# Kernel optimization log

Measured on AMD Instinct MI355X. Metric: run time of the kernel, lower is better.

The kernel has to match this reference:

```python
import jax, jax.numpy as jnp
import numpy as np
from functools import partial

EPS = 1e-10


@partial(jax.custom_vjp, nondiff_argnums=(1,))
def kwta(x, k):
    # k-WTA: keep top-k values along last dim, zero elsewhere (STE backward).
    vals, _ = jax.lax.top_k(x, k)
    thresh = vals[..., -1:]
    return jnp.where(x >= thresh, x, jnp.zeros((), x.dtype))


def _kwta_fwd(x, k):
    out = kwta(x, k)
    mask = (out != 0).astype(x.dtype)  # matches torch: mask = (out != 0)
    return out, mask


def _kwta_bwd(k, mask, g):
    return (g * mask,)


kwta.defvjp(_kwta_fwd, _kwta_bwd)


def _sparsify(x, W_down, k):
    h = jax.nn.relu(x @ W_down.T)          # (B, T, N_ca3)
    h = kwta(h, k)
    norm = jnp.maximum(jnp.linalg.norm(h, axis=-1, keepdims=True), EPS)
    return h / norm


def _retrieve_successor(sparse, W_ca3, k):
    # retrieval_steps = 1; replicate the early-break on all-zero activity.
    h = jax.nn.relu(sparse @ W_ca3.T)       # (B, T, N_ca3)
    valid = h.sum() >= EPS
    hk = kwta(h, k)
    norm = jnp.maximum(jnp.linalg.norm(hk, axis=-1, keepdims=True), EPS)
    return jnp.where(valid, hk / norm, sparse)


def setup_inputs() -> dict:
    key = jax.random.key(0)
    k1, k2, k3, k4, k5, k6 = jax.random.split(key, 6)
    B, T, D, N = 4, 2048, 1024, 4096
    x = jax.random.normal(k1, (B, T, D), dtype=jnp.float32)
    # xavier_normal: std = gain * sqrt(2 / (fan_in + fan_out))
    W_down = jax.random.normal(k2, (N, D), dtype=jnp.float32) * (0.5 * np.sqrt(2.0 / (D + N)))
    W_up = jax.random.normal(k3, (D, N), dtype=jnp.float32) * (0.1 * np.sqrt(2.0 / (D + N)))
    # gate_proj weight is zero-init in torch; use small random for a nontrivial gate
    W_gate = jax.random.normal(k4, (D, D), dtype=jnp.float32) * 0.02
    b_gate = jnp.full((D,), -2.0, dtype=jnp.float32)
    # W_ca3 buffer is zero-init then Hebbian-learned; random stand-in
    W_ca3 = jax.random.normal(k6, (N, N), dtype=jnp.float32) * 0.02
    return {"x": x, "W_down": W_down, "W_up": W_up, "W_gate": W_gate,
            "b_gate": b_gate, "W_ca3": W_ca3, "k": 64}


def reference(x, W_down, W_up, W_gate, b_gate, W_ca3, k):
    sparse = _sparsify(x, W_down, k)                    # (B, T, N)
    successor = _retrieve_successor(sparse, W_ca3, k)   # (B, T, N)
    prediction = successor @ W_up.T                     # (B, T, D)
    g = jax.nn.sigmoid(x @ W_gate.T + b_gate)           # (B, T, D)
    return x + g * prediction
```

## Files before the change

kernel.cpp:

```cpp
#include <hip/hip_runtime.h>
#include <hip/hip_bf16.h>
#include <stdint.h>

typedef float f32x4 __attribute__((ext_vector_type(4)));
typedef int i32x4 __attribute__((ext_vector_type(4)));

#define MROWS 8192
#define DD 1024
#define DN 4096

__device__ __forceinline__ void load_lds16(const void* g, void* l) {
  __builtin_amdgcn_global_load_lds((const __attribute__((address_space(1))) void*)g,
                                   (__attribute__((address_space(3))) void*)l, 16, 0, 0);
}

template<int EPI>
__global__ void __launch_bounds__(512, 1)
gemm_i8_8ph(const uint8_t* __restrict__ A, const uint8_t* __restrict__ B,
            __hip_bfloat16* __restrict__ Cb, int M, int N, int K,
            float* __restrict__ vsum,
            const float* __restrict__ sA, const float* __restrict__ sB)
{
  extern __shared__ __align__(16) char smem[];
  const int tid  = threadIdx.x;
  const int lane = tid & 63;
  const int wave = tid >> 6;
  const int wm = wave >> 2;
  const int wn = wave & 3;

  const int nwg = gridDim.x;
  const int bid = ((int)blockIdx.x % 8) * (nwg >> 3) + ((int)blockIdx.x >> 3);

  const int nbn = N >> 8;
  const int bm = (bid / nbn) << 8;
  const int bn = (bid % nbn) << 8;

  const int NT = K >> 7;

  i32x4 acc[8][4];
  const i32x4 izero = {0, 0, 0, 0};
#pragma unroll
  for (int i = 0; i < 8; ++i)
#pragma unroll
    for (int j = 0; j < 4; ++j)
      acc[i][j] = izero;

  const int csb = (((tid & 3) ^ ((tid >> 3) & 3)) << 4);
  const uint8_t* Ag = A + (size_t)(bm + (tid >> 2)) * K + csb;
  const uint8_t* Bg = B + (size_t)(bn + (tid >> 2)) * K + csb;

  const int rl = lane & 15;
  const int kc = lane >> 4;
  const int chunk_off = ((kc ^ ((rl >> 1) & 3)) << 4);
  const int aoff = ((wm << 7) + rl) * 64 + chunk_off;
  const int boff = ((wn << 6) + rl) * 64 + chunk_off;

#define STAGE_A8(S, KH) do { \
    const int kt_ = (((S) & (NT - 1)) << 7) + ((KH) << 6); \
    char* dst_ = smem + (((((S) & 1) << 1) | (KH)) << 14) + (tid << 4); \
    load_lds16(Ag + kt_, dst_); \
    load_lds16(Ag + (size_t)128 * K + kt_, dst_ + 8192); \
  } while (0)

#define STAGE_B8(S, KH) do { \
    const int kt_ = (((S) & (NT - 1)) << 7) + ((KH) << 6); \
    char* dst_ = smem + 65536 + (((((S) & 1) << 1) | (KH)) << 14) + (tid << 4); \
    load_lds16(Bg + kt_, dst_); \
    load_lds16(Bg + (size_t)128 * K + kt_, dst_ + 8192); \
  } while (0)

  i32x4 afS[2][4];
  i32x4 b0, b1, b2, b3;

#define MFMA_ROW8(MI, AF) \
    acc[MI][0] = __builtin_amdgcn_mfma_i32_16x16x64_i8(AF, b0, acc[MI][0], 0, 0, 0); \
    acc[MI][1] = __builtin_amdgcn_mfma_i32_16x16x64_i8(AF, b1, acc[MI][1], 0, 0, 0); \
    acc[MI][2] = __builtin_amdgcn_mfma_i32_16x16x64_i8(AF, b2, acc[MI][2], 0, 0, 0); \
    acc[MI][3] = __builtin_amdgcn_mfma_i32_16x16x64_i8(AF, b3, acc[MI][3], 0, 0, 0);

#define PH8(PN, KHN, MHN, ASETN, ACUR, MHC, DOBP, BP, BKH, STG, VM) do { \
    { const char* ab_ = smem + ((((PN) << 1) | (KHN)) << 14) + aoff + (MHN) * 4096; \
      afS[ASETN][0] = *(const i32x4*)(ab_); \
      afS[ASETN][1] = *(const i32x4*)(ab_ + 1024); \
      afS[ASETN][2] = *(const i32x4*)(ab_ + 2048); \
      afS[ASETN][3] = *(const i32x4*)(ab_ + 3072); } \
    STG; \
    if (VM) { asm volatile("s_waitcnt vmcnt(6)" ::: "memory"); } \
    asm volatile("s_barrier" ::: "memory"); \
    __builtin_amdgcn_sched_barrier(0); \
    __builtin_amdgcn_s_setprio(1); \
    MFMA_ROW8((MHC) * 4 + 0, afS[ACUR][0]) \
    MFMA_ROW8((MHC) * 4 + 1, afS[ACUR][1]) \
    MFMA_ROW8((MHC) * 4 + 2, afS[ACUR][2]) \
    MFMA_ROW8((MHC) * 4 + 3, afS[ACUR][3]) \
    __builtin_amdgcn_s_setprio(0); \
    if (DOBP) { \
      const char* bb_ = smem + 65536 + ((((BP) << 1) | (BKH)) << 14) + boff; \
      b0 = *(const i32x4*)(bb_); b1 = *(const i32x4*)(bb_ + 1024); \
      b2 = *(const i32x4*)(bb_ + 2048); b3 = *(const i32x4*)(bb_ + 3072); } \
    asm volatile("s_barrier" ::: "memory"); \
  } while (0)

  STAGE_A8(0, 0); STAGE_B8(0, 0);
  STAGE_A8(0, 1); STAGE_B8(0, 1);
  STAGE_A8(1, 0); STAGE_B8(1, 0);
  asm volatile("s_waitcnt vmcnt(4)" ::: "memory");
  asm volatile("s_barrier" ::: "memory");
  {
    const char* ab_ = smem + aoff;
    afS[1][0] = *(const i32x4*)(ab_);
    afS[1][1] = *(const i32x4*)(ab_ + 1024);
    afS[1][2] = *(const i32x4*)(ab_ + 2048);
    afS[1][3] = *(const i32x4*)(ab_ + 3072);
    const char* bb_ = smem + 65536 + boff;
    b0 = *(const i32x4*)(bb_); b1 = *(const i32x4*)(bb_ + 1024);
    b2 = *(const i32x4*)(bb_ + 2048); b3 = *(const i32x4*)(bb_ + 3072);
  }

#pragma unroll 1
  for (int t = 0; t < NT; t += 2) {
    PH8(0, 0, 1, 0, 1, 0, 0, 0, 0, STAGE_A8(t + 1, 1), 1);
    PH8(0, 1, 0, 1, 0, 1, 1, 0, 1, STAGE_B8(t + 1, 1), 0);
    PH8(0, 1, 1, 0, 1, 0, 0, 0, 0, STAGE_A8(t + 2, 0), 1);
    PH8(1, 0, 0, 1, 0, 1, 1, 1, 0, STAGE_B8(t + 2, 0), 0);
    PH8(1, 0, 1, 0, 1, 0, 0, 0, 0, STAGE_A8(t + 2, 1), 1);
    PH8(1, 1, 0, 1, 0, 1, 1, 1, 1, STAGE_B8(t + 2, 1), 0);
    PH8(1, 1, 1, 0, 1, 0, 0, 0, 0, STAGE_A8(t + 3, 0), 1);
    PH8(0, 0, 0, 1, 0, 1, 1, 0, 0, STAGE_B8(t + 3, 0), 0);
  }

  const int r0 = bm + (wm << 7) + (kc << 2);
  const int c0 = bn + (wn << 6) + rl;
  float lsum = 0.f;
#pragma unroll
  for (int mi = 0; mi < 8; ++mi) {
#pragma unroll
    for (int nf = 0; nf < 4; ++nf) {
#pragma unroll
      for (int q = 0; q < 4; ++q) {
        const int r = r0 + (mi << 4) + q;
        const int c = c0 + (nf << 4);
        float v = (float)acc[mi][nf][q] * sA[r] * sB[c];
        v = fmaxf(v, 0.f);
        Cb[(size_t)r * N + c] = __float2bfloat16(v);
        if constexpr (EPI == 1) lsum += v;
      }
    }
  }
  if constexpr (EPI == 1) {
#pragma unroll
    for (int off = 32; off > 0; off >>= 1)
      lsum += __shfl_down(lsum, off);
    if (lane == 0) atomicAdd(vsum, lsum);
  }

#undef STAGE_A8
#undef STAGE_B8
#undef MFMA_ROW8
#undef PH8
}

__global__ void __launch_bounds__(256)
gemm_predgate(const uint8_t* __restrict__ Asp, const uint8_t* __restrict__ Bup,
              const uint8_t* __restrict__ Ax,  const uint8_t* __restrict__ Bg8,
              float* __restrict__ Cf, int M, int N, int K1, int K2,
              const float* __restrict__ sA,  const float* __restrict__ swu,
              const float* __restrict__ sx,  const float* __restrict__ swg,
              const float* __restrict__ Xf,  const float* __restrict__ Bgate)
{
  __shared__ __align__(16) char smem[32768];
  const int tid  = threadIdx.x;
  const int lane = tid & 63;
  const int wave = tid >> 6;

  const int nbn = N >> 7;
  const int bm = ((int)blockIdx.x / nbn) << 7;
  const int bn = ((int)blockIdx.x % nbn) << 7;

  const int wm = (wave >> 1) << 6;
  const int wn = (wave & 1) << 6;

  i32x4 acc1[4][4], acc2[4][4];
  const i32x4 izero = {0, 0, 0, 0};
#pragma unroll
  for (int i = 0; i < 4; ++i)
#pragma unroll
    for (int j = 0; j < 4; ++j) { acc1[i][j] = izero; acc2[i][j] = izero; }

  const int srow = tid >> 3;
  const int schk = (tid & 7) ^ (srow & 7);
  char* ldsA = smem + (wave << 10);
  char* ldsB = smem + 16384 + (wave << 10);

  const int aoff0 = (wm + (lane & 15)) << 7;
  const int boff0 = 16384 + ((wn + (lane & 15)) << 7);
  const int kc = lane >> 4;
  const int sw = lane & 7;

#define K_LOOP(APTR, BPTR, KK, ACC) do { \
    const uint8_t* Ag = (APTR) + (size_t)(bm + srow) * (KK) + (schk << 4); \
    const uint8_t* Bg = (BPTR) + (size_t)(bn + srow) * (KK) + (schk << 4); \
    for (int k0 = 0; k0 < (KK); k0 += 128) { \
      _Pragma("unroll") \
      for (int i = 0; i < 4; ++i) \
        load_lds16(Ag + (size_t)(i << 5) * (KK) + k0, ldsA + (i << 12)); \
      _Pragma("unroll") \
      for (int i = 0; i < 4; ++i) \
        load_lds16(Bg + (size_t)(i << 5) * (KK) + k0, ldsB + (i << 12)); \
      __syncthreads(); \
      _Pragma("unroll") \
      for (int ks = 0; ks < 2; ++ks) { \
        const int cb = ((kc + (ks << 2)) ^ sw) << 4; \
        i32x4 af[4], bfr[4]; \
        _Pragma("unroll") \
        for (int i = 0; i < 4; ++i) \
          af[i] = *reinterpret_cast<const i32x4*>(smem + aoff0 + (i << 11) + cb); \
        _Pragma("unroll") \
        for (int j = 0; j < 4; ++j) \
          bfr[j] = *reinterpret_cast<const i32x4*>(smem + boff0 + (j << 11) + cb); \
        _Pragma("unroll") \
        for (int i = 0; i < 4; ++i) \
          _Pragma("unroll") \
          for (int j = 0; j < 4; ++j) \
            ACC[i][j] = __builtin_amdgcn_mfma_i32_16x16x64_i8(af[i], bfr[j], ACC[i][j], 0, 0, 0); \
      } \
      __syncthreads(); \
    } \
  } while (0)

  K_LOOP(Asp, Bup, K1, acc1);
  K_LOOP(Ax,  Bg8, K2, acc2);
#undef K_LOOP

  const int r0 = bm + wm + ((lane >> 4) << 2);
  const int c0 = bn + wn + (lane & 15);
#pragma unroll
  for (int i = 0; i < 4; ++i) {
#pragma unroll
    for (int j = 0; j < 4; ++j) {
#pragma unroll
      for (int q = 0; q < 4; ++q) {
        const int r = r0 + (i << 4) + q;
        const int c = c0 + (j << 4);
        const size_t idx = (size_t)r * N + c;
        const float pred = (float)acc1[i][j][q] * sA[r] * swu[c];
        const float vg   = (float)acc2[i][j][q] * sx[r] * swg[c] + Bgate[c];
        const float g = 1.f / (1.f + __expf(-vg));
        Cf[idx] = Xf[idx] + g * pred;
      }
    }
  }
}

template<int MODE>
__global__ void __launch_bounds__(256)
kwta_wave(const __hip_bfloat16* __restrict__ H, uint8_t* __restrict__ OUTQ,
          float* __restrict__ sA, const float* __restrict__ vsumPtr,
          const int* __restrict__ kptr)
{
  const int tid  = threadIdx.x;
  const int lane = tid & 63;
  const int w    = tid >> 6;
  const int row  = ((int)blockIdx.x << 2) + w;

  if constexpr (MODE == 1) {
    if (!(*vsumPtr >= 1e-10f)) return;
  }

  const uint4* h8 = (const uint4*)(H + (size_t)row * 4096);
  uint4 d[8];
#pragma unroll
  for (int i = 0; i < 8; ++i) d[i] = h8[(i << 6) + lane];

  const unsigned k = (unsigned)(*kptr);

  unsigned kmax = 0;
#pragma unroll
  for (int i = 0; i < 8; ++i) {
    const unsigned* p = (const unsigned*)&d[i];
#pragma unroll
    for (int c4 = 0; c4 < 4; ++c4) {
      kmax = max(kmax, p[c4] & 0xffffu);
      kmax = max(kmax, p[c4] >> 16);
    }
  }
#pragma unroll
  for (int off = 32; off > 0; off >>= 1) kmax = max(kmax, __shfl_xor(kmax, off));

  unsigned lo = 0, hi = 65536;
#pragma unroll 1
  for (int it = 0; it < 16; ++it) {
    const unsigned mid = (lo + hi) >> 1;
    unsigned c = 0;
#pragma unroll
    for (int i = 0; i < 8; ++i) {
      const unsigned* p = (const unsigned*)&d[i];
#pragma unroll
      for (int c4 = 0; c4 < 4; ++c4) {
        c += ((p[c4] & 0xffffu) >= mid) ? 1u : 0u;
        c += ((p[c4] >> 16) >= mid) ? 1u : 0u;
      }
    }
#pragma unroll
    for (int off = 32; off > 0; off >>= 1) c += __shfl_xor(c, off);
    if (c >= k) lo = mid; else hi = mid;
  }
  const unsigned threshKey = lo;

  float ss = 0.f;
#pragma unroll
  for (int i = 0; i < 8; ++i) {
    const unsigned* p = (const unsigned*)&d[i];
#pragma unroll
    for (int c4 = 0; c4 < 4; ++c4) {
#pragma unroll
      for (int hh = 0; hh < 2; ++hh) {
        const unsigned key = hh ? (p[c4] >> 16) : (p[c4] & 0xffffu);
        if (key >= threshKey) {
          const float v = __uint_as_float(key << 16);
          ss = fmaf(v, v, ss);
        }
      }
    }
  }
#pragma unroll
  for (int off = 32; off > 0; off >>= 1) ss += __shfl_xor(ss, off);
  const float inv = 1.f / fmaxf(sqrtf(ss), 1e-10f);

  const float vmaxf = __uint_as_float(kmax << 16);
  const float r127 = (kmax > 0) ? 127.f / vmaxf : 0.f;

  if (lane == 0) sA[row] = vmaxf * inv * (1.f / 127.f);

  uint2* o2 = (uint2*)(OUTQ + (size_t)row * 4096);
#pragma unroll
  for (int i = 0; i < 8; ++i) {
    const unsigned* p = (const unsigned*)&d[i];
    unsigned b[8];
#pragma unroll
    for (int c4 = 0; c4 < 4; ++c4) {
#pragma unroll
      for (int hh = 0; hh < 2; ++hh) {
        const unsigned key = hh ? (p[c4] >> 16) : (p[c4] & 0xffffu);
        unsigned q = 0;
        if (key >= threshKey && key > 0) {
          const float v = __uint_as_float(key << 16);
          q = (unsigned)__float2int_rn(v * r127) & 0xffu;
        }
        b[c4 * 2 + hh] = q;
      }
    }
    uint2 o;
    o.x = b[0] | (b[1] << 8) | (b[2] << 16) | (b[3] << 24);
    o.y = b[4] | (b[5] << 8) | (b[6] << 16) | (b[7] << 24);
    o2[(i << 6) + lane] = o;
  }
}

__global__ void __launch_bounds__(256)
quant1024(const float* __restrict__ X, const float* __restrict__ Wd,
          const float* __restrict__ Wg,
          uint8_t* __restrict__ xq, uint8_t* __restrict__ wdq,
          uint8_t* __restrict__ wgq,
          float* __restrict__ sx, float* __restrict__ swd,
          float* __restrict__ swg)
{
  const int wgl = ((int)blockIdx.x << 2) + (threadIdx.x >> 6);
  const int lane = threadIdx.x & 63;

  const float* W; uint8_t* q; float* s; int row;
  if      (wgl < 8192)  { W = X;  q = xq;  s = sx;  row = wgl; }
  else if (wgl < 12288) { W = Wd; q = wdq; s = swd; row = wgl - 8192; }
  else                  { W = Wg; q = wgq; s = swg; row = wgl - 12288; }

  const float4* src = (const float4*)(W + (size_t)row * 1024);
  float4 v[4];
  float am = 0.f;
#pragma unroll
  for (int i = 0; i < 4; ++i) {
    v[i] = src[(i << 6) + lane];
    am = fmaxf(am, fmaxf(fmaxf(fabsf(v[i].x), fabsf(v[i].y)),
                         fmaxf(fabsf(v[i].z), fabsf(v[i].w))));
  }
#pragma unroll
  for (int off = 32; off > 0; off >>= 1) am = fmaxf(am, __shfl_xor(am, off));

  const float rinv = (am > 0.f) ? 127.f / am : 0.f;
  uint4 o;
  unsigned* ob = (unsigned*)&o;
#pragma unroll
  for (int i = 0; i < 4; ++i) {
    const unsigned b0 = (unsigned)__float2int_rn(v[i].x * rinv) & 0xffu;
    const unsigned b1 = (unsigned)__float2int_rn(v[i].y * rinv) & 0xffu;
    const unsigned b2 = (unsigned)__float2int_rn(v[i].z * rinv) & 0xffu;
    const unsigned b3 = (unsigned)__float2int_rn(v[i].w * rinv) & 0xffu;
    ob[i] = b0 | (b1 << 8) | (b2 << 16) | (b3 << 24);
  }
  ((uint4*)(q + (size_t)row * 1024))[lane] = o;
  if (lane == 0) s[row] = am * (1.f / 127.f);
}

__global__ void __launch_bounds__(256)
quant4096(const float* __restrict__ Wc, const float* __restrict__ Wu,
          uint8_t* __restrict__ qc, uint8_t* __restrict__ qu,
          float* __restrict__ sc, float* __restrict__ su)
{
  const int wgl = ((int)blockIdx.x << 2) + (threadIdx.x >> 6);
  const int lane = threadIdx.x & 63;

  const float* W; uint8_t* q; float* s; int row;
  if (wgl < 4096) { W = Wc; q = qc; s = sc; row = wgl; }
  else            { W = Wu; q = qu; s = su; row = wgl - 4096; }

  const float4* src = (const float4*)(W + (size_t)row * 4096);
  float4 v[16];
  float am = 0.f;
#pragma unroll
  for (int i = 0; i < 16; ++i) {
    v[i] = src[(i << 6) + lane];
    am = fmaxf(am, fmaxf(fmaxf(fabsf(v[i].x), fabsf(v[i].y)),
                         fmaxf(fabsf(v[i].z), fabsf(v[i].w))));
  }
#pragma unroll
  for (int off = 32; off > 0; off >>= 1) am = fmaxf(am, __shfl_xor(am, off));

  const float rinv = (am > 0.f) ? 127.f / am : 0.f;
  unsigned* qo = (unsigned*)(q + (size_t)row * 4096);
#pragma unroll
  for (int i = 0; i < 16; ++i) {
    const unsigned b0 = (unsigned)__float2int_rn(v[i].x * rinv) & 0xffu;
    const unsigned b1 = (unsigned)__float2int_rn(v[i].y * rinv) & 0xffu;
    const unsigned b2 = (unsigned)__float2int_rn(v[i].z * rinv) & 0xffu;
    const unsigned b3 = (unsigned)__float2int_rn(v[i].w * rinv) & 0xffu;
    qo[(i << 6) + lane] = b0 | (b1 << 8) | (b2 << 16) | (b3 << 24);
  }
  if (lane == 0) s[row] = am * (1.f / 127.f);
}

__global__ void diag_kernel(float* out, float mb)
{
  if (threadIdx.x == 0 && blockIdx.x == 0) out[0] = -mb;
}

extern "C" void kernel_launch(void* const* d_in, const int* in_sizes, int n_in,
                              void* d_out, int out_size, void* d_ws, size_t ws_size,
                              hipStream_t stream)
{
  const float* x     = (const float*)d_in[0];
  const float* Wdown = (const float*)d_in[1];
  const float* Wup   = (const float*)d_in[2];
  const float* Wgate = (const float*)d_in[3];
  const float* bgate = (const float*)d_in[4];
  const float* Wca3  = (const float*)d_in[5];
  const int*   kptr  = (const int*)d_in[6];

  const size_t OFF_XQ   = 0;
  const size_t OFF_WDQ  = 8388608;
  const size_t OFF_WGQ  = 12582912;
  const size_t OFF_WCQ  = 13631488;
  const size_t OFF_WUQ  = 30408704;
  const size_t OFF_SX   = 34603008;
  const size_t OFF_SWD  = 34635776;
  const size_t OFF_SWG  = 34652160;
  const size_t OFF_SWC  = 34656256;
  const size_t OFF_SWU  = 34672640;
  const size_t OFF_SA   = 34676736;
  const size_t OFF_VSUM = 34709504;
  const size_t OFF_SPQ  = 34713600;
  const size_t OFF_H    = 68268032;
  const size_t NEED     = 135376896;

  if (ws_size < NEED) {
    diag_kernel<<<1, 64, 0, stream>>>((float*)d_out, (float)(ws_size >> 20));
    return;
  }

  char* ws = (char*)d_ws;
  uint8_t*        xq   = (uint8_t*)       (ws + OFF_XQ);
  uint8_t*        wdq  = (uint8_t*)       (ws + OFF_WDQ);
  uint8_t*        wgq  = (uint8_t*)       (ws + OFF_WGQ);
  uint8_t*        wcq  = (uint8_t*)       (ws + OFF_WCQ);
  uint8_t*        wuq  = (uint8_t*)       (ws + OFF_WUQ);
  float*          sx   = (float*)         (ws + OFF_SX);
  float*          swd  = (float*)         (ws + OFF_SWD);
  float*          swg  = (float*)         (ws + OFF_SWG);
  float*          swc  = (float*)         (ws + OFF_SWC);
  float*          swu  = (float*)         (ws + OFF_SWU);
  float*          sA   = (float*)         (ws + OFF_SA);
  float*          vsum = (float*)         (ws + OFF_VSUM);
  uint8_t*        spq  = (uint8_t*)       (ws + OFF_SPQ);
  __hip_bfloat16* h    = (__hip_bfloat16*)(ws + OFF_H);

  hipMemsetAsync(vsum, 0, sizeof(float), stream);

  quant1024<<<3328, 256, 0, stream>>>(x, Wdown, Wgate, xq, wdq, wgq, sx, swd, swg);
  quant4096<<<1280, 256, 0, stream>>>(Wca3, Wup, wcq, wuq, swc, swu);

  gemm_i8_8ph<0><<<(MROWS >> 8) * (DN >> 8), 512, 131072, stream>>>(
      xq, wdq, h, MROWS, DN, DD, nullptr, sx, swd);
  kwta_wave<0><<<MROWS / 4, 256, 0, stream>>>(h, spq, sA, nullptr, kptr);
  gemm_i8_8ph<1><<<(MROWS >> 8) * (DN >> 8), 512, 131072, stream>>>(
      spq, wcq, h, MROWS, DN, DN, vsum, sA, swc);
  kwta_wave<1><<<MROWS / 4, 256, 0, stream>>>(h, spq, sA, vsum, kptr);
  gemm_predgate<<<(MROWS >> 7) * (DD >> 7), 256, 0, stream>>>(
      spq, wuq, xq, wgq, (float*)d_out, MROWS, DD, DN, DD,
      sA, swu, sx, swg, x, bgate);
}
```

Baseline: 457.5 us.

## Split fused pred/gate GEMM into two kernels, merge quant launches, add XCD-aware block remap

Replaces the fused prediction+gate GEMM with two kernels. The first writes the prediction in bf16 to the h workspace. The second runs the gate GEMM and combines it with x and the stored prediction. Both kernels remap block IDs across 8 groups, which likely targets L2 locality per XCD, and the two quantization kernels are merged into one launch. This lowers register pressure from the dual accumulators and cuts launch count, at the cost of an extra bf16 round-trip through memory and bf16 rounding of the prediction.

New measurement: 406.3 us. -11.2%, faster.

```diff
diff --git a/kernel.cpp b/kernel.cpp
--- a/kernel.cpp
+++ b/kernel.cpp
@@ -161,34 +161,37 @@
 }
 
 __global__ void __launch_bounds__(256)
-gemm_predgate(const uint8_t* __restrict__ Asp, const uint8_t* __restrict__ Bup,
-              const uint8_t* __restrict__ Ax,  const uint8_t* __restrict__ Bg8,
-              float* __restrict__ Cf, int M, int N, int K1, int K2,
-              const float* __restrict__ sA,  const float* __restrict__ swu,
-              const float* __restrict__ sx,  const float* __restrict__ swg,
-              const float* __restrict__ Xf,  const float* __restrict__ Bgate)
+gemm_i8_128(const uint8_t* __restrict__ A, const uint8_t* __restrict__ B,
+            __hip_bfloat16* __restrict__ Cb, int M, int N, int K,
+            const float* __restrict__ sA, const float* __restrict__ sB)
 {
   __shared__ __align__(16) char smem[32768];
   const int tid  = threadIdx.x;
   const int lane = tid & 63;
   const int wave = tid >> 6;
 
+  const int nwg = gridDim.x;
+  const int bid = ((int)blockIdx.x % 8) * (nwg >> 3) + ((int)blockIdx.x >> 3);
+
   const int nbn = N >> 7;
-  const int bm = ((int)blockIdx.x / nbn) << 7;
-  const int bn = ((int)blockIdx.x % nbn) << 7;
+  const int bm = (bid / nbn) << 7;
+  const int bn = (bid % nbn) << 7;
 
   const int wm = (wave >> 1) << 6;
   const int wn = (wave & 1) << 6;
 
-  i32x4 acc1[4][4], acc2[4][4];
+  i32x4 acc[4][4];
   const i32x4 izero = {0, 0, 0, 0};
 #pragma unroll
   for (int i = 0; i < 4; ++i)
 #pragma unroll
-    for (int j = 0; j < 4; ++j) { acc1[i][j] = izero; acc2[i][j] = izero; }
+    for (int j = 0; j < 4; ++j)
+      acc[i][j] = izero;
 
   const int srow = tid >> 3;
   const int schk = (tid & 7) ^ (srow & 7);
+  const uint8_t* Ag = A + (size_t)(bm + srow) * K + (schk << 4);
+  const uint8_t* Bg = B + (size_t)(bn + srow) * K + (schk << 4);
   char* ldsA = smem + (wave << 10);
   char* ldsB = smem + 16384 + (wave << 10);
 
@@ -197,59 +200,131 @@
   const int kc = lane >> 4;
   const int sw = lane & 7;
 
-#define K_LOOP(APTR, BPTR, KK, ACC) do { \
-    const uint8_t* Ag = (APTR) + (size_t)(bm + srow) * (KK) + (schk << 4); \
-    const uint8_t* Bg = (BPTR) + (size_t)(bn + srow) * (KK) + (schk << 4); \
-    for (int k0 = 0; k0 < (KK); k0 += 128) { \
-      _Pragma("unroll") \
-      for (int i = 0; i < 4; ++i) \
-        load_lds16(Ag + (size_t)(i << 5) * (KK) + k0, ldsA + (i << 12)); \
-      _Pragma("unroll") \
-      for (int i = 0; i < 4; ++i) \
-        load_lds16(Bg + (size_t)(i << 5) * (KK) + k0, ldsB + (i << 12)); \
-      __syncthreads(); \
-      _Pragma("unroll") \
-      for (int ks = 0; ks < 2; ++ks) { \
-        const int cb = ((kc + (ks << 2)) ^ sw) << 4; \
-        i32x4 af[4], bfr[4]; \
-        _Pragma("unroll") \
-        for (int i = 0; i < 4; ++i) \
-          af[i] = *reinterpret_cast<const i32x4*>(smem + aoff0 + (i << 11) + cb); \
-        _Pragma("unroll") \
-        for (int j = 0; j < 4; ++j) \
-          bfr[j] = *reinterpret_cast<const i32x4*>(smem + boff0 + (j << 11) + cb); \
-        _Pragma("unroll") \
-        for (int i = 0; i < 4; ++i) \
-          _Pragma("unroll") \
-          for (int j = 0; j < 4; ++j) \
-            ACC[i][j] = __builtin_amdgcn_mfma_i32_16x16x64_i8(af[i], bfr[j], ACC[i][j], 0, 0, 0); \
-      } \
-      __syncthreads(); \
-    } \
-  } while (0)
-
-  K_LOOP(Asp, Bup, K1, acc1);
-  K_LOOP(Ax,  Bg8, K2, acc2);
-#undef K_LOOP
+  for (int k0 = 0; k0 < K; k0 += 128) {
+#pragma unroll
+    for (int i = 0; i < 4; ++i)
+      load_lds16(Ag + (size_t)(i << 5) * K + k0, ldsA + (i << 12));
+#pragma unroll
+    for (int i = 0; i < 4; ++i)
+      load_lds16(Bg + (size_t)(i << 5) * K + k0, ldsB + (i << 12));
+    __syncthreads();
+#pragma unroll
+    for (int ks = 0; ks < 2; ++ks) {
+      const int cb = ((kc + (ks << 2)) ^ sw) << 4;
+      i32x4 af[4], bfr[4];
+#pragma unroll
+      for (int i = 0; i < 4; ++i)
+        af[i] = *reinterpret_cast<const i32x4*>(smem + aoff0 + (i << 11) + cb);
+#pragma unroll
+      for (int j = 0; j < 4; ++j)
+        bfr[j] = *reinterpret_cast<const i32x4*>(smem + boff0 + (j << 11) + cb);
+#pragma unroll
+      for (int i = 0; i < 4; ++i)
+#pragma unroll
+        for (int j = 0; j < 4; ++j)
+          acc[i][j] = __builtin_amdgcn_mfma_i32_16x16x64_i8(af[i], bfr[j], acc[i][j], 0, 0, 0);
+    }
+    __syncthreads();
+  }
 
   const int r0 = bm + wm + ((lane >> 4) << 2);
   const int c0 = bn + wn + (lane & 15);
 #pragma unroll
-  for (int i = 0; i < 4; ++i) {
-#pragma unroll
-    for (int j = 0; j < 4; ++j) {
+  for (int i = 0; i < 4; ++i)
+#pragma unroll
+    for (int j = 0; j < 4; ++j)
+#pragma unroll
+      for (int q = 0; q < 4; ++q) {
+        const int r = r0 + (i << 4) + q;
+        const int c = c0 + (j << 4);
+        Cb[(size_t)r * N + c] =
+            __float2bfloat16((float)acc[i][j][q] * sA[r] * sB[c]);
+      }
+}
+
+__global__ void __launch_bounds__(256)
+gemm_gate_i8(const uint8_t* __restrict__ A, const uint8_t* __restrict__ B,
+             float* __restrict__ Cf, int M, int N, int K,
+             const float* __restrict__ sA, const float* __restrict__ sB,
+             const float* __restrict__ Xf, const __hip_bfloat16* __restrict__ PredBf,
+             const float* __restrict__ Bgate)
+{
+  __shared__ __align__(16) char smem[32768];
+  const int tid  = threadIdx.x;
+  const int lane = tid & 63;
+  const int wave = tid >> 6;
+
+  const int nwg = gridDim.x;
+  const int bid = ((int)blockIdx.x % 8) * (nwg >> 3) + ((int)blockIdx.x >> 3);
+
+  const int nbn = N >> 7;
+  const int bm = (bid / nbn) << 7;
+  const int bn = (bid % nbn) << 7;
+
+  const int wm = (wave >> 1) << 6;
+  const int wn = (wave & 1) << 6;
+
+  i32x4 acc[4][4];
+  const i32x4 izero = {0, 0, 0, 0};
+#pragma unroll
+  for (int i = 0; i < 4; ++i)
+#pragma unroll
+    for (int j = 0; j < 4; ++j) acc[i][j] = izero;
+
+  const int srow = tid >> 3;
+  const int schk = (tid & 7) ^ (srow & 7);
+  const uint8_t* Ag = A + (size_t)(bm + srow) * K + (schk << 4);
+  const uint8_t* Bg = B + (size_t)(bn + srow) * K + (schk << 4);
+  char* ldsA = smem + (wave << 10);
+  char* ldsB = smem + 16384 + (wave << 10);
+
+  const int aoff0 = (wm + (lane & 15)) << 7;
+  const int boff0 = 16384 + ((wn + (lane & 15)) << 7);
+  const int kc = lane >> 4;
+  const int sw = lane & 7;
+
+  for (int k0 = 0; k0 < K; k0 += 128) {
+#pragma unroll
+    for (int i = 0; i < 4; ++i)
+      load_lds16(Ag + (size_t)(i << 5) * K + k0, ldsA + (i << 12));
+#pragma unroll
+    for (int i = 0; i < 4; ++i)
+      load_lds16(Bg + (size_t)(i << 5) * K + k0, ldsB + (i << 12));
+    __syncthreads();
+#pragma unroll
+    for (int ks = 0; ks < 2; ++ks) {
+      const int cb = ((kc + (ks << 2)) ^ sw) << 4;
+      i32x4 af[4], bfr[4];
+#pragma unroll
+      for (int i = 0; i < 4; ++i)
+        af[i] = *reinterpret_cast<const i32x4*>(smem + aoff0 + (i << 11) + cb);
+#pragma unroll
+      for (int j = 0; j < 4; ++j)
+        bfr[j] = *reinterpret_cast<const i32x4*>(smem + boff0 + (j << 11) + cb);
+#pragma unroll
+      for (int i = 0; i < 4; ++i)
+#pragma unroll
+        for (int j = 0; j < 4; ++j)
+          acc[i][j] = __builtin_amdgcn_mfma_i32_16x16x64_i8(af[i], bfr[j], acc[i][j], 0, 0, 0);
+    }
+    __syncthreads();
+  }
+
+  const int r0 = bm + wm + ((lane >> 4) << 2);
+  const int c0 = bn + wn + (lane & 15);
+#pragma unroll
+  for (int i = 0; i < 4; ++i)
+#pragma unroll
+    for (int j = 0; j < 4; ++j)
 #pragma unroll
       for (int q = 0; q < 4; ++q) {
         const int r = r0 + (i << 4) + q;
         const int c = c0 + (j << 4);
         const size_t idx = (size_t)r * N + c;
-        const float pred = (float)acc1[i][j][q] * sA[r] * swu[c];
-        const float vg   = (float)acc2[i][j][q] * sx[r] * swg[c] + Bgate[c];
+        const float vg = (float)acc[i][j][q] * sA[r] * sB[c] + Bgate[c];
         const float g = 1.f / (1.f + __expf(-vg));
-        Cf[idx] = Xf[idx] + g * pred;
+        Cf[idx] = Xf[idx] + g * __bfloat162float(PredBf[idx]);
       }
-    }
-  }
 }
 
 template<int MODE>
@@ -358,83 +433,75 @@
 }
 
 __global__ void __launch_bounds__(256)
-quant1024(const float* __restrict__ X, const float* __restrict__ Wd,
-          const float* __restrict__ Wg,
-          uint8_t* __restrict__ xq, uint8_t* __restrict__ wdq,
-          uint8_t* __restrict__ wgq,
-          float* __restrict__ sx, float* __restrict__ swd,
-          float* __restrict__ swg)
+quant_all(const float* __restrict__ X,  const float* __restrict__ Wd,
+          const float* __restrict__ Wg, const float* __restrict__ Wc,
+          const float* __restrict__ Wu,
+          uint8_t* __restrict__ xq,  uint8_t* __restrict__ wdq,
+          uint8_t* __restrict__ wgq, uint8_t* __restrict__ wcq,
+          uint8_t* __restrict__ wuq,
+          float* __restrict__ sx,  float* __restrict__ swd,
+          float* __restrict__ swg, float* __restrict__ swc,
+          float* __restrict__ swu)
 {
   const int wgl = ((int)blockIdx.x << 2) + (threadIdx.x >> 6);
   const int lane = threadIdx.x & 63;
 
-  const float* W; uint8_t* q; float* s; int row;
-  if      (wgl < 8192)  { W = X;  q = xq;  s = sx;  row = wgl; }
-  else if (wgl < 12288) { W = Wd; q = wdq; s = swd; row = wgl - 8192; }
-  else                  { W = Wg; q = wgq; s = swg; row = wgl - 12288; }
-
-  const float4* src = (const float4*)(W + (size_t)row * 1024);
-  float4 v[4];
-  float am = 0.f;
-#pragma unroll
-  for (int i = 0; i < 4; ++i) {
-    v[i] = src[(i << 6) + lane];
-    am = fmaxf(am, fmaxf(fmaxf(fabsf(v[i].x), fabsf(v[i].y)),
-                         fmaxf(fabsf(v[i].z), fabsf(v[i].w))));
-  }
-#pragma unroll
-  for (int off = 32; off > 0; off >>= 1) am = fmaxf(am, __shfl_xor(am, off));
-
-  const float rinv = (am > 0.f) ? 127.f / am : 0.f;
-  uint4 o;
-  unsigned* ob = (unsigned*)&o;
-#pragma unroll
-  for (int i = 0; i < 4; ++i) {
-    const unsigned b0 = (unsigned)__float2int_rn(v[i].x * rinv) & 0xffu;
-    const unsigned b1 = (unsigned)__float2int_rn(v[i].y * rinv) & 0xffu;
-    const unsigned b2 = (unsigned)__float2int_rn(v[i].z * rinv) & 0xffu;
-    const unsigned b3 = (unsigned)__float2int_rn(v[i].w * rinv) & 0xffu;
-    ob[i] = b0 | (b1 << 8) | (b2 << 16) | (b3 << 24);
-  }
-  ((uint4*)(q + (size_t)row * 1024))[lane] = o;
-  if (lane == 0) s[row] = am * (1.f / 127.f);
-}
-
-__global__ void __launch_bounds__(256)
-quant4096(const float* __restrict__ Wc, const float* __restrict__ Wu,
-          uint8_t* __restrict__ qc, uint8_t* __restrict__ qu,
-          float* __restrict__ sc, float* __restrict__ su)
-{
-  const int wgl = ((int)blockIdx.x << 2) + (threadIdx.x >> 6);
-  const int lane = threadIdx.x & 63;
-
-  const float* W; uint8_t* q; float* s; int row;
-  if (wgl < 4096) { W = Wc; q = qc; s = sc; row = wgl; }
-  else            { W = Wu; q = qu; s = su; row = wgl - 4096; }
-
-  const float4* src = (const float4*)(W + (size_t)row * 4096);
-  float4 v[16];
-  float am = 0.f;
-#pragma unroll
-  for (int i = 0; i < 16; ++i) {
-    v[i] = src[(i << 6) + lane];
-    am = fmaxf(am, fmaxf(fmaxf(fabsf(v[i].x), fabsf(v[i].y)),
-                         fmaxf(fabsf(v[i].z), fabsf(v[i].w))));
-  }
-#pragma unroll
-  for (int off = 32; off > 0; off >>= 1) am = fmaxf(am, __shfl_xor(am, off));
-
-  const float rinv = (am > 0.f) ? 127.f / am : 0.f;
-  unsigned* qo = (unsigned*)(q + (size_t)row * 4096);
-#pragma unroll
-  for (int i = 0; i < 16; ++i) {
-    const unsigned b0 = (unsigned)__float2int_rn(v[i].x * rinv) & 0xffu;
-    const unsigned b1 = (unsigned)__float2int_rn(v[i].y * rinv) & 0xffu;
-    const unsigned b2 = (unsigned)__float2int_rn(v[i].z * rinv) & 0xffu;
-    const unsigned b3 = (unsigned)__float2int_rn(v[i].w * rinv) & 0xffu;
-    qo[(i << 6) + lane] = b0 | (b1 << 8) | (b2 << 16) | (b3 << 24);
-  }
-  if (lane == 0) s[row] = am * (1.f / 127.f);
+  const float* W; uint8_t* q; float* s; int row; bool big;
+  if      (wgl < 8192)  { W = X;  q = xq;  s = sx;  row = wgl;         big = false; }
+  else if (wgl < 12288) { W = Wd; q = wdq; s = swd; row = wgl - 8192;  big = false; }
+  else if (wgl < 13312) { W = Wg; q = wgq; s = swg; row = wgl - 12288; big = false; }
+  else if (wgl < 17408) { W = Wc; q = wcq; s = swc; row = wgl - 13312; big = true; }
+  else                  { W = Wu; q = wuq; s = swu; row = wgl - 17408; big = true; }
+
+  if (!big) {
+    const float4* src = (const float4*)(W + (size_t)row * 1024);
+    float4 v[4];
+    float am = 0.f;
+#pragma unroll
+    for (int i = 0; i < 4; ++i) {
+      v[i] = src[(i << 6) + lane];
+      am = fmaxf(am, fmaxf(fmaxf(fabsf(v[i].x), fabsf(v[i].y)),
+                           fmaxf(fabsf(v[i].z), fabsf(v[i].w))));
+    }
+#pragma unroll
+    for (int off = 32; off > 0; off >>= 1) am = fmaxf(am, __shfl_xor(am, off));
+    const float rinv = (am > 0.f) ? 127.f / am : 0.f;
+    uint4 o;
+    unsigned* ob = (unsigned*)&o;
+#pragma unroll
+    for (int i = 0; i < 4; ++i) {
+      const unsigned b0 = (unsigned)__float2int_rn(v[i].x * rinv) & 0xffu;
+      const unsigned b1 = (unsigned)__float2int_rn(v[i].y * rinv) & 0xffu;
+      const unsigned b2 = (unsigned)__float2int_rn(v[i].z * rinv) & 0xffu;
+      const unsigned b3 = (unsigned)__float2int_rn(v[i].w * rinv) & 0xffu;
+      ob[i] = b0 | (b1 << 8) | (b2 << 16) | (b3 << 24);
+    }
+    ((uint4*)(q + (size_t)row * 1024))[lane] = o;
+    if (lane == 0) s[row] = am * (1.f / 127.f);
+  } else {
+    const float4* src = (const float4*)(W + (size_t)row * 4096);
+    float4 v[16];
+    float am = 0.f;
+#pragma unroll
+    for (int i = 0; i < 16; ++i) {
+      v[i] = src[(i << 6) + lane];
+      am = fmaxf(am, fmaxf(fmaxf(fabsf(v[i].x), fabsf(v[i].y)),
+                           fmaxf(fabsf(v[i].z), fabsf(v[i].w))));
+    }
+#pragma unroll
+    for (int off = 32; off > 0; off >>= 1) am = fmaxf(am, __shfl_xor(am, off));
+    const float rinv = (am > 0.f) ? 127.f / am : 0.f;
+    unsigned* qo = (unsigned*)(q + (size_t)row * 4096);
+#pragma unroll
+    for (int i = 0; i < 16; ++i) {
+      const unsigned b0 = (unsigned)__float2int_rn(v[i].x * rinv) & 0xffu;
+      const unsigned b1 = (unsigned)__float2int_rn(v[i].y * rinv) & 0xffu;
+      const unsigned b2 = (unsigned)__float2int_rn(v[i].z * rinv) & 0xffu;
+      const unsigned b3 = (unsigned)__float2int_rn(v[i].w * rinv) & 0xffu;
+      qo[(i << 6) + lane] = b0 | (b1 << 8) | (b2 << 16) | (b3 << 24);
+    }
+    if (lane == 0) s[row] = am * (1.f / 127.f);
+  }
 }
 
 __global__ void diag_kernel(float* out, float mb)
@@ -490,11 +557,13 @@
   float*          vsum = (float*)         (ws + OFF_VSUM);
   uint8_t*        spq  = (uint8_t*)       (ws + OFF_SPQ);
   __hip_bfloat16* h    = (__hip_bfloat16*)(ws + OFF_H);
+  __hip_bfloat16* pred = (__hip_bfloat16*)(ws + OFF_H);
 
   hipMemsetAsync(vsum, 0, sizeof(float), stream);
 
-  quant1024<<<3328, 256, 0, stream>>>(x, Wdown, Wgate, xq, wdq, wgq, sx, swd, swg);
-  quant4096<<<1280, 256, 0, stream>>>(Wca3, Wup, wcq, wuq, swc, swu);
+  quant_all<<<4608, 256, 0, stream>>>(x, Wdown, Wgate, Wca3, Wup,
+                                      xq, wdq, wgq, wcq, wuq,
+                                      sx, swd, swg, swc, swu);
 
   gemm_i8_8ph<0><<<(MROWS >> 8) * (DN >> 8), 512, 131072, stream>>>(
       xq, wdq, h, MROWS, DN, DD, nullptr, sx, swd);
@@ -502,7 +571,8 @@
   gemm_i8_8ph<1><<<(MROWS >> 8) * (DN >> 8), 512, 131072, stream>>>(
       spq, wcq, h, MROWS, DN, DN, vsum, sA, swc);
   kwta_wave<1><<<MROWS / 4, 256, 0, stream>>>(h, spq, sA, vsum, kptr);
-  gemm_predgate<<<(MROWS >> 7) * (DD >> 7), 256, 0, stream>>>(
-      spq, wuq, xq, wgq, (float*)d_out, MROWS, DD, DN, DD,
-      sA, swu, sx, swg, x, bgate);
-}
+  gemm_i8_128<<<(MROWS >> 7) * (DD >> 7), 256, 0, stream>>>(
+      spq, wuq, pred, MROWS, DD, DN, sA, swu);
+  gemm_gate_i8<<<(MROWS >> 7) * (DD >> 7), 256, 0, stream>>>(
+      xq, wgq, (float*)d_out, MROWS, DD, DD, sx, swg, x, pred, bgate);
+}
```
